# Performance work log

Hardware: AMD Instinct MI355X
Metric: run time of the kernel (lower is better)

## Reference

```python
import jax, jax.numpy as jnp
import numpy as np

N_NODES = 100000


def _gcn_norm(edge_index, num_nodes):
    # PyG gcn_norm with add_self_loops=True, symmetric normalization.
    src = jnp.concatenate([edge_index[0], jnp.arange(num_nodes)])
    dst = jnp.concatenate([edge_index[1], jnp.arange(num_nodes)])
    ones = jnp.ones(src.shape[0], dtype=jnp.float32)
    deg = jax.ops.segment_sum(ones, dst, num_segments=num_nodes)
    dinv = jnp.where(deg > 0, jax.lax.rsqrt(deg), 0.0)
    norm = dinv[src] * dinv[dst]  # [E + N]
    return src, dst, norm


def _gcn_conv(x, W, b, src, dst, norm, num_nodes):
    h = x @ W                                  # dense transform first (PyG order)
    msg = h[src] * norm[:, None]               # gather + scale, [E+N, D]
    agg = jax.ops.segment_sum(msg, dst, num_segments=num_nodes)
    return agg + b


def setup_inputs() -> dict:
    key = jax.random.key(0)
    ks = jax.random.split(key, 6)
    F_in, D, C, E = 256, 64, 47, 1200000
    x = jax.random.normal(ks[0], (N_NODES, F_in), dtype=jnp.float32)
    edge_index = jax.random.randint(ks[1], (2, E), 0, N_NODES)
    W1 = jax.random.normal(ks[2], (F_in, D), dtype=jnp.float32) * (1.0 / np.sqrt(F_in))
    b1 = jnp.zeros((D,), dtype=jnp.float32)
    W2 = jax.random.normal(ks[3], (D, C), dtype=jnp.float32) * (1.0 / np.sqrt(D))
    b2 = jnp.zeros((C,), dtype=jnp.float32)
    return {"x": x, "edge_index": edge_index, "W1": W1, "b1": b1, "W2": W2, "b2": b2}


def reference(x, edge_index, W1, b1, W2, b2):
    src, dst, norm = _gcn_norm(edge_index, N_NODES)
    h = jax.nn.relu(_gcn_conv(x, W1, b1, src, dst, norm, N_NODES))
    # dropout: eval mode (training=False) -> identity
    out = _gcn_conv(h, W2, b2, src, dst, norm, N_NODES)
    return jax.nn.log_softmax(out, axis=1)
```

## Files before the change

kernel.cpp:

```cpp
#include <hip/hip_runtime.h>
#include <math.h>

#define NN 100000
#define FIN 256
#define D1 64
#define C2 47
#define S2 48
#define PREPB 76
#define NBKT 1563
#define CAP 1024
#define EPB 4096

typedef unsigned short u16;
typedef unsigned int u32;
typedef __attribute__((ext_vector_type(8))) short short8;
typedef __attribute__((ext_vector_type(4))) float floatx4;

__device__ __forceinline__ u16 f2b(float f) {
    union { float f; unsigned u; } v; v.f = f;
    unsigned r = v.u + 0x7FFF + ((v.u >> 16) & 1);
    return (u16)(r >> 16);
}
__device__ __forceinline__ float b2f_lo(u32 p) { union { unsigned u; float f; } v; v.u = p << 16; return v.f; }
__device__ __forceinline__ float b2f_hi(u32 p) { union { unsigned u; float f; } v; v.u = p & 0xFFFF0000u; return v.f; }

__global__ __launch_bounds__(256) void k_prep_bucket(
    const float* __restrict__ W1, const float* __restrict__ W2,
    u16* __restrict__ W1t, u16* __restrict__ W2t,
    const int* __restrict__ src, const int* __restrict__ dst, int E,
    int* __restrict__ bucketCnt, u32* __restrict__ ebuf)
{
    int b = blockIdx.x;
    if (b < PREPB) {
        int i = b * 256 + threadIdx.x;
        if (i < FIN * D1) {
            int c = i >> 8, k = i & 255;
            W1t[i] = f2b(W1[k * D1 + c]);
        } else if (i < FIN * D1 + D1 * S2) {
            int j = i - FIN * D1;
            int c = j >> 6, k = j & 63;
            W2t[j] = (c < C2) ? f2b(W2[k * C2 + c]) : (u16)0;
        }
        return;
    }
    __shared__ int hist[NBKT];
    __shared__ int base[NBKT];
    const int t = threadIdx.x;
    const int blk = b - PREPB;
    for (int i = t; i < NBKT; i += 256) hist[i] = 0;
    __syncthreads();

    int e0 = blk * EPB + t;
    u32 pk[16]; int bk[16], tk[16];
    #pragma unroll
    for (int j = 0; j < 16; ++j) {
        int e = e0 + j * 256;
        bk[j] = -1;
        if (e < E) {
            int d = dst[e];
            bk[j] = d >> 6;
            pk[j] = (u32)src[e] | ((u32)(d & 63) << 17);
            tk[j] = atomicAdd(&hist[bk[j]], 1);
        }
    }
    __syncthreads();
    for (int i = t; i < NBKT; i += 256)
        base[i] = hist[i] ? atomicAdd(&bucketCnt[i], hist[i]) : 0;
    __syncthreads();
    #pragma unroll
    for (int j = 0; j < 16; ++j)
        if (bk[j] >= 0) {
            int pos = base[bk[j]] + tk[j];
            if (pos < CAP) ebuf[(size_t)bk[j] * CAP + pos] = pk[j];
        }
}

__global__ __launch_bounds__(256) void k_gemm1(
    const int* __restrict__ bucketCnt, const u32* __restrict__ ebuf,
    const float* __restrict__ x, const u16* __restrict__ W1t,
    float* __restrict__ dinv, int* __restrict__ rpg, u32* __restrict__ sortedg,
    u16* __restrict__ hs1)
{
    __shared__ short As[2][64 * 40];
    __shared__ short Bs[2][64 * 40];
    __shared__ int hist[64], cur[64];
    __shared__ float dinvs[64];
    const int b = blockIdx.x;
    const int t = threadIdx.x;
    const int bm = b * 64;

    if (t < 64) hist[t] = 0;
    __syncthreads();
    int cnt = bucketCnt[b]; if (cnt > CAP) cnt = CAP;
    const u32* eb = ebuf + (size_t)b * CAP;
    for (int i = t; i < cnt; i += 256)
        atomicAdd(&hist[(eb[i] >> 17) & 63], 1);
    __syncthreads();
    if (t < 64) {
        int h = hist[t];
        int v = h;
        #pragma unroll
        for (int off = 1; off < 64; off <<= 1) {
            int u = __shfl_up(v, off);
            if (t >= off) v += u;
        }
        cur[t] = v - h;
        rpg[(size_t)b * 64 + t] = v - h;
        float dv = rsqrtf((float)h + 1.0f);
        dinvs[t] = dv;
        dinv[bm + t] = dv;
    }
    __syncthreads();
    for (int i = t; i < cnt; i += 256) {
        u32 p = eb[i];
        int pos = atomicAdd(&cur[(p >> 17) & 63], 1);
        sortedg[(size_t)b * CAP + pos] = p & 0x1FFFF;
    }

    const int w = t >> 6, lane = t & 63;
    const int arow = t >> 2;
    const int ak0 = (t & 3) * 8;

    floatx4 acc[4] = {};
    const int gr = bm + arow;
    const bool rowok = gr < NN;
    const float* xrow = x + (size_t)(rowok ? gr : 0) * FIN + ak0;

    float4 v0 = make_float4(0.f,0.f,0.f,0.f), v1 = v0;
    if (rowok) { v0 = *(const float4*)(xrow); v1 = *(const float4*)(xrow + 4); }
    short8 wv = *(const short8*)(W1t + arow * FIN + ak0);
    {
        short8 av;
        av[0]=(short)f2b(v0.x); av[1]=(short)f2b(v0.y); av[2]=(short)f2b(v0.z); av[3]=(short)f2b(v0.w);
        av[4]=(short)f2b(v1.x); av[5]=(short)f2b(v1.y); av[6]=(short)f2b(v1.z); av[7]=(short)f2b(v1.w);
        *(short8*)(&As[0][arow * 40 + ak0]) = av;
        *(short8*)(&Bs[0][arow * 40 + ak0]) = wv;
    }
    __syncthreads();

    int cb_ = 0;
    for (int kt = 32; kt <= FIN; kt += 32) {
        const bool more = kt < FIN;
        float4 n0, n1; short8 nw;
        if (more) {
            if (rowok) { n0 = *(const float4*)(xrow + kt); n1 = *(const float4*)(xrow + kt + 4); }
            else { n0 = make_float4(0.f,0.f,0.f,0.f); n1 = n0; }
            nw = *(const short8*)(W1t + arow * FIN + kt + ak0);
        }
        short8 af = *(const short8*)(&As[cb_][(w * 16 + (lane & 15)) * 40 + (lane >> 4) * 8]);
        #pragma unroll
        for (int cb = 0; cb < 4; ++cb) {
            short8 bv = *(const short8*)(&Bs[cb_][(cb * 16 + (lane & 15)) * 40 + (lane >> 4) * 8]);
            acc[cb] = __builtin_amdgcn_mfma_f32_16x16x32_bf16(af, bv, acc[cb], 0, 0, 0);
        }
        if (!more) break;
        short8 av;
        av[0]=(short)f2b(n0.x); av[1]=(short)f2b(n0.y); av[2]=(short)f2b(n0.z); av[3]=(short)f2b(n0.w);
        av[4]=(short)f2b(n1.x); av[5]=(short)f2b(n1.y); av[6]=(short)f2b(n1.z); av[7]=(short)f2b(n1.w);
        *(short8*)(&As[cb_ ^ 1][arow * 40 + ak0]) = av;
        *(short8*)(&Bs[cb_ ^ 1][arow * 40 + ak0]) = nw;
        __syncthreads();
        cb_ ^= 1;
    }

    #pragma unroll
    for (int cb = 0; cb < 4; ++cb) {
        #pragma unroll
        for (int r = 0; r < 4; ++r) {
            int rl = w * 16 + (lane >> 4) * 4 + r;
            int grow = bm + rl;
            if (grow < NN) {
                float v = acc[cb][r] * dinvs[rl];
                hs1[(size_t)grow * D1 + cb * 16 + (lane & 15)] = f2b(v);
            }
        }
    }
}

__global__ __launch_bounds__(256) void k_gather_gemm2(
    const int* __restrict__ bucketCnt, const int* __restrict__ rpg,
    const u32* __restrict__ sortedg,
    const float* __restrict__ dinv, const u16* __restrict__ hs1,
    const float* __restrict__ b1, const u16* __restrict__ W2t,
    u16* __restrict__ hs2)
{
    __shared__ u32 sorted[CAP];
    __shared__ int rp[65];
    __shared__ short As[2][64 * 40];
    __shared__ short Bs[2][48 * 40];
    __shared__ float dinvs[64];
    __shared__ float b1s[64];
    const int t = threadIdx.x;
    const int b = blockIdx.x, bm = b * 64;
    const int w = t >> 6, lane = t & 63;
    const int g = t >> 3, l8 = t & 7;

    for (int s = t; s < 384; s += 256) {
        int kt = s / 192, rem = s - kt * 192;
        int r = rem >> 2, j = rem & 3;
        *(short8*)(&Bs[kt][r * 40 + j * 8]) =
            *(const short8*)(W2t + r * D1 + kt * 32 + j * 8);
    }
    int cnt = bucketCnt[b]; if (cnt > CAP) cnt = CAP;
    if (t < 64) { dinvs[t] = dinv[bm + t]; b1s[t] = b1[t]; rp[t] = rpg[(size_t)b * 64 + t]; }
    if (t == 0) rp[64] = cnt;
    for (int i = t; i < cnt; i += 256)
        sorted[i] = sortedg[(size_t)b * CAP + i];
    __syncthreads();

    {
        const int col = 8 * l8;
        const int kth = l8 >> 2;
        const int cs  = col & 31;
        float4 bbl = *(const float4*)(b1s + col);
        float4 bbh = *(const float4*)(b1s + col + 4);
        #pragma unroll 1
        for (int i = 0; i < 2; ++i) {
            int rl = g * 2 + i;
            int node = bm + rl;
            if (node >= NN) break;
            int beg = rp[rl], end = rp[rl + 1];
            uint4 sp = *((const uint4*)(hs1 + (size_t)node * D1) + l8);
            float a0=b2f_lo(sp.x), a1=b2f_hi(sp.x), a2=b2f_lo(sp.y), a3=b2f_hi(sp.y);
            float a4=b2f_lo(sp.z), a5=b2f_hi(sp.z), a6=b2f_lo(sp.w), a7=b2f_hi(sp.w);
            float c0=0.f,c1=0.f,c2=0.f,c3=0.f,c4=0.f,c5=0.f,c6=0.f,c7=0.f;
            int e = beg;
            for (; e + 4 <= end; e += 4) {
                int s0 = sorted[e+0], s1 = sorted[e+1], s2 = sorted[e+2], s3 = sorted[e+3];
                uint4 p0 = *((const uint4*)(hs1 + (size_t)s0 * D1) + l8);
                uint4 p1 = *((const uint4*)(hs1 + (size_t)s1 * D1) + l8);
                uint4 p2 = *((const uint4*)(hs1 + (size_t)s2 * D1) + l8);
                uint4 p3 = *((const uint4*)(hs1 + (size_t)s3 * D1) + l8);
                a0+=b2f_lo(p0.x); a1+=b2f_hi(p0.x); a2+=b2f_lo(p0.y); a3+=b2f_hi(p0.y);
                a4+=b2f_lo(p0.z); a5+=b2f_hi(p0.z); a6+=b2f_lo(p0.w); a7+=b2f_hi(p0.w);
                c0+=b2f_lo(p1.x); c1+=b2f_hi(p1.x); c2+=b2f_lo(p1.y); c3+=b2f_hi(p1.y);
                c4+=b2f_lo(p1.z); c5+=b2f_hi(p1.z); c6+=b2f_lo(p1.w); c7+=b2f_hi(p1.w);
                a0+=b2f_lo(p2.x); a1+=b2f_hi(p2.x); a2+=b2f_lo(p2.y); a3+=b2f_hi(p2.y);
                a4+=b2f_lo(p2.z); a5+=b2f_hi(p2.z); a6+=b2f_lo(p2.w); a7+=b2f_hi(p2.w);
                c0+=b2f_lo(p3.x); c1+=b2f_hi(p3.x); c2+=b2f_lo(p3.y); c3+=b2f_hi(p3.y);
                c4+=b2f_lo(p3.z); c5+=b2f_hi(p3.z); c6+=b2f_lo(p3.w); c7+=b2f_hi(p3.w);
            }
            for (; e < end; ++e) {
                uint4 p0 = *((const uint4*)(hs1 + (size_t)sorted[e] * D1) + l8);
                a0+=b2f_lo(p0.x); a1+=b2f_hi(p0.x); a2+=b2f_lo(p0.y); a3+=b2f_hi(p0.y);
                a4+=b2f_lo(p0.z); a5+=b2f_hi(p0.z); a6+=b2f_lo(p0.w); a7+=b2f_hi(p0.w);
            }
            float dd = dinvs[rl];
            float r0 = fmaxf(fmaf(dd, a0 + c0, bbl.x), 0.f);
            float r1 = fmaxf(fmaf(dd, a1 + c1, bbl.y), 0.f);
            float r2 = fmaxf(fmaf(dd, a2 + c2, bbl.z), 0.f);
            float r3 = fmaxf(fmaf(dd, a3 + c3, bbl.w), 0.f);
            float r4 = fmaxf(fmaf(dd, a4 + c4, bbh.x), 0.f);
            float r5 = fmaxf(fmaf(dd, a5 + c5, bbh.y), 0.f);
            float r6 = fmaxf(fmaf(dd, a6 + c6, bbh.z), 0.f);
            float r7 = fmaxf(fmaf(dd, a7 + c7, bbh.w), 0.f);
            short8 pk;
            pk[0]=(short)f2b(r0); pk[1]=(short)f2b(r1); pk[2]=(short)f2b(r2); pk[3]=(short)f2b(r3);
            pk[4]=(short)f2b(r4); pk[5]=(short)f2b(r5); pk[6]=(short)f2b(r6); pk[7]=(short)f2b(r7);
            *(short8*)(&As[kth][rl * 40 + cs]) = pk;
        }
    }
    __syncthreads();

    floatx4 acc2[3] = {};
    #pragma unroll
    for (int kt = 0; kt < 2; ++kt) {
        short8 af = *(const short8*)(&As[kt][(w * 16 + (lane & 15)) * 40 + (lane >> 4) * 8]);
        #pragma unroll
        for (int cb = 0; cb < 3; ++cb) {
            short8 bv = *(const short8*)(&Bs[kt][(cb * 16 + (lane & 15)) * 40 + (lane >> 4) * 8]);
            acc2[cb] = __builtin_amdgcn_mfma_f32_16x16x32_bf16(af, bv, acc2[cb], 0, 0, 0);
        }
    }

    #pragma unroll
    for (int cb = 0; cb < 3; ++cb) {
        #pragma unroll
        for (int r = 0; r < 4; ++r) {
            int rl2 = w * 16 + (lane >> 4) * 4 + r;
            int grow = bm + rl2;
            if (grow < NN) {
                float v = acc2[cb][r] * dinvs[rl2];
                hs2[(size_t)grow * S2 + cb * 16 + (lane & 15)] = f2b(v);
            }
        }
    }
}

__global__ __launch_bounds__(256) void k_gather47(
    const int* __restrict__ bucketCnt, const int* __restrict__ rpg,
    const u32* __restrict__ sortedg,
    const float* __restrict__ dinv, const u16* __restrict__ hs2,
    const float* __restrict__ b2, float* __restrict__ out)
{
    __shared__ u32 sorted[CAP];
    __shared__ int rp[65];
    __shared__ float dinvs[64];
    __shared__ float b2s[48];
    const int t = threadIdx.x;
    const int b = blockIdx.x, bm = b * 64;
    const int g = t >> 3, l8 = t & 7;

    int cnt = bucketCnt[b]; if (cnt > CAP) cnt = CAP;
    if (t < 64) { dinvs[t] = dinv[bm + t]; rp[t] = rpg[(size_t)b * 64 + t]; }
    if (t < 48) b2s[t] = (t < C2) ? b2[t] : 0.f;
    if (t == 0) rp[64] = cnt;
    for (int i = t; i < cnt; i += 256)
        sorted[i] = sortedg[(size_t)b * CAP + i];
    __syncthreads();

    const bool act = l8 < 6;
    const int lc = act ? l8 : 0;
    #pragma unroll 1
    for (int i = 0; i < 2; ++i) {
        int rl = g * 2 + i;
        int node = bm + rl;
        if (node >= NN) break;
        int beg = rp[rl], end = rp[rl + 1];
        uint4 sp = *((const uint4*)(hs2 + (size_t)node * S2) + lc);
        float a0=b2f_lo(sp.x), a1=b2f_hi(sp.x), a2=b2f_lo(sp.y), a3=b2f_hi(sp.y);
        float a4=b2f_lo(sp.z), a5=b2f_hi(sp.z), a6=b2f_lo(sp.w), a7=b2f_hi(sp.w);
        float c0=0.f,c1=0.f,c2=0.f,c3=0.f,c4=0.f,c5=0.f,c6=0.f,c7=0.f;
        int e = beg;
        for (; e + 4 <= end; e += 4) {
            int s0 = sorted[e+0], s1 = sorted[e+1], s2 = sorted[e+2], s3 = sorted[e+3];
            uint4 p0 = *((const uint4*)(hs2 + (size_t)s0 * S2) + lc);
            uint4 p1 = *((const uint4*)(hs2 + (size_t)s1 * S2) + lc);
            uint4 p2 = *((const uint4*)(hs2 + (size_t)s2 * S2) + lc);
            uint4 p3 = *((const uint4*)(hs2 + (size_t)s3 * S2) + lc);
            a0+=b2f_lo(p0.x); a1+=b2f_hi(p0.x); a2+=b2f_lo(p0.y); a3+=b2f_hi(p0.y);
            a4+=b2f_lo(p0.z); a5+=b2f_hi(p0.z); a6+=b2f_lo(p0.w); a7+=b2f_hi(p0.w);
            c0+=b2f_lo(p1.x); c1+=b2f_hi(p1.x); c2+=b2f_lo(p1.y); c3+=b2f_hi(p1.y);
            c4+=b2f_lo(p1.z); c5+=b2f_hi(p1.z); c6+=b2f_lo(p1.w); c7+=b2f_hi(p1.w);
            a0+=b2f_lo(p2.x); a1+=b2f_hi(p2.x); a2+=b2f_lo(p2.y); a3+=b2f_hi(p2.y);
            a4+=b2f_lo(p2.z); a5+=b2f_hi(p2.z); a6+=b2f_lo(p2.w); a7+=b2f_hi(p2.w);
            c0+=b2f_lo(p3.x); c1+=b2f_hi(p3.x); c2+=b2f_lo(p3.y); c3+=b2f_hi(p3.y);
            c4+=b2f_lo(p3.z); c5+=b2f_hi(p3.z); c6+=b2f_lo(p3.w); c7+=b2f_hi(p3.w);
        }
        for (; e < end; ++e) {
            uint4 p0 = *((const uint4*)(hs2 + (size_t)sorted[e] * S2) + lc);
            a0+=b2f_lo(p0.x); a1+=b2f_hi(p0.x); a2+=b2f_lo(p0.y); a3+=b2f_hi(p0.y);
            a4+=b2f_lo(p0.z); a5+=b2f_hi(p0.z); a6+=b2f_lo(p0.w); a7+=b2f_hi(p0.w);
        }
        float dd = dinvs[rl];
        float fv[8] = { a0+c0, a1+c1, a2+c2, a3+c3, a4+c4, a5+c5, a6+c6, a7+c7 };
        const int fb = 8 * lc;
        float val[8];
        float m = -INFINITY;
        #pragma unroll
        for (int k = 0; k < 8; ++k) {
            int fe = fb + k;
            bool valid = act && (fe < C2);
            val[k] = valid ? fmaf(dd, fv[k], b2s[valid ? fe : 0]) : -INFINITY;
            m = fmaxf(m, val[k]);
        }
        #pragma unroll
        for (int off = 1; off < 8; off <<= 1) m = fmaxf(m, __shfl_xor(m, off));
        float ex = 0.f;
        #pragma unroll
        for (int k = 0; k < 8; ++k)
            if (val[k] > -INFINITY) ex += expf(val[k] - m);
        #pragma unroll
        for (int off = 1; off < 8; off <<= 1) ex += __shfl_xor(ex, off);
        float ls = m + logf(ex);
        #pragma unroll
        for (int k = 0; k < 8; ++k) {
            int fe = fb + k;
            if (act && fe < C2) out[(size_t)node * C2 + fe] = val[k] - ls;
        }
    }
}

extern "C" void kernel_launch(void* const* d_in, const int* in_sizes, int n_in,
                              void* d_out, int out_size, void* d_ws, size_t ws_size,
                              hipStream_t stream) {
    const float* x  = (const float*)d_in[0];
    const int*   ei = (const int*)d_in[1];
    const float* W1 = (const float*)d_in[2];
    const float* b1 = (const float*)d_in[3];
    const float* W2 = (const float*)d_in[4];
    const float* b2 = (const float*)d_in[5];
    float* out = (float*)d_out;

    const int E = in_sizes[1] / 2;
    const int* src = ei;
    const int* dst = ei + E;

    char* ws = (char*)d_ws;
    float* dinv      = (float*)(ws);
    int*   bucketCnt = (int*)(ws + 0x80000);
    u16*   W1t       = (u16*)(ws + 0x180000);
    u16*   W2t       = (u16*)(ws + 0x189000);
    int*   rpg       = (int*)(ws + 0x190000);
    u32*   ebuf      = (u32*)(ws + 0x200000);
    u32*   sortedg   = (u32*)(ws + 0x900000);
    u16*   hs1       = (u16*)(ws + 0x1000000);
    u16*   hs2       = (u16*)(ws + 0x1E00000);

    const int nBk1 = (E + EPB - 1) / EPB;

    hipMemsetAsync(bucketCnt, 0, NBKT * sizeof(int), stream);
    k_prep_bucket<<<PREPB + nBk1, 256, 0, stream>>>(W1, W2, W1t, W2t, src, dst, E,
                                                    bucketCnt, ebuf);
    k_gemm1<<<NBKT, 256, 0, stream>>>(bucketCnt, ebuf, x, W1t, dinv, rpg, sortedg, hs1);
    k_gather_gemm2<<<NBKT, 256, 0, stream>>>(bucketCnt, rpg, sortedg, dinv, hs1, b1, W2t, hs2);
    k_gather47<<<NBKT, 256, 0, stream>>>(bucketCnt, rpg, sortedg, dinv, hs2, b2, out);
}
```

Before: 124.3 us.

## Overlap edge binning with GEMM1 and move degree scaling into a sort kernel

The edge bucket scatter now runs in the same launch as the dense x@W1 GEMM, so the two independent phases can overlap across CUs. The memset is folded into the weight-prep kernel. Because the GEMM no longer waits on degrees, it writes unscaled h1 and a new sort/scale kernel rescales it by dinv. Downstream kernels recompute dinv from row-pointer counts instead of reading a dinv array. The cost is an extra launch and an extra read and write pass over h1.

```diff
diff --git a/kernel.cpp b/kernel.cpp
--- a/kernel.cpp
+++ b/kernel.cpp
@@ -6,7 +6,6 @@
 #define D1 64
 #define C2 47
 #define S2 48
-#define PREPB 76
 #define NBKT 1563
 #define CAP 1024
 #define EPB 4096
@@ -23,100 +22,72 @@
 }
 __device__ __forceinline__ float b2f_lo(u32 p) { union { unsigned u; float f; } v; v.u = p << 16; return v.f; }
 __device__ __forceinline__ float b2f_hi(u32 p) { union { unsigned u; float f; } v; v.u = p & 0xFFFF0000u; return v.f; }
-
-__global__ __launch_bounds__(256) void k_prep_bucket(
+__device__ __forceinline__ u32 scale2(u32 pair, float dd) {
+    return (u32)f2b(dd * b2f_lo(pair)) | ((u32)f2b(dd * b2f_hi(pair)) << 16);
+}
+
+__global__ __launch_bounds__(256) void k_pre(
     const float* __restrict__ W1, const float* __restrict__ W2,
-    u16* __restrict__ W1t, u16* __restrict__ W2t,
-    const int* __restrict__ src, const int* __restrict__ dst, int E,
-    int* __restrict__ bucketCnt, u32* __restrict__ ebuf)
+    u16* __restrict__ W1t, u16* __restrict__ W2t, int* __restrict__ bucketCnt)
 {
-    int b = blockIdx.x;
-    if (b < PREPB) {
-        int i = b * 256 + threadIdx.x;
-        if (i < FIN * D1) {
-            int c = i >> 8, k = i & 255;
-            W1t[i] = f2b(W1[k * D1 + c]);
-        } else if (i < FIN * D1 + D1 * S2) {
-            int j = i - FIN * D1;
-            int c = j >> 6, k = j & 63;
-            W2t[j] = (c < C2) ? f2b(W2[k * C2 + c]) : (u16)0;
-        }
-        return;
-    }
-    __shared__ int hist[NBKT];
-    __shared__ int base[NBKT];
-    const int t = threadIdx.x;
-    const int blk = b - PREPB;
-    for (int i = t; i < NBKT; i += 256) hist[i] = 0;
-    __syncthreads();
-
-    int e0 = blk * EPB + t;
-    u32 pk[16]; int bk[16], tk[16];
-    #pragma unroll
-    for (int j = 0; j < 16; ++j) {
-        int e = e0 + j * 256;
-        bk[j] = -1;
-        if (e < E) {
-            int d = dst[e];
-            bk[j] = d >> 6;
-            pk[j] = (u32)src[e] | ((u32)(d & 63) << 17);
-            tk[j] = atomicAdd(&hist[bk[j]], 1);
-        }
-    }
-    __syncthreads();
-    for (int i = t; i < NBKT; i += 256)
-        base[i] = hist[i] ? atomicAdd(&bucketCnt[i], hist[i]) : 0;
-    __syncthreads();
-    #pragma unroll
-    for (int j = 0; j < 16; ++j)
-        if (bk[j] >= 0) {
-            int pos = base[bk[j]] + tk[j];
-            if (pos < CAP) ebuf[(size_t)bk[j] * CAP + pos] = pk[j];
-        }
-}
-
-__global__ __launch_bounds__(256) void k_gemm1(
-    const int* __restrict__ bucketCnt, const u32* __restrict__ ebuf,
+    int i = blockIdx.x * 256 + threadIdx.x;
+    if (i < FIN * D1) {
+        int c = i >> 8, k = i & 255;
+        W1t[i] = f2b(W1[k * D1 + c]);
+    } else if (i < FIN * D1 + D1 * S2) {
+        int j = i - FIN * D1;
+        int c = j >> 6, k = j & 63;
+        W2t[j] = (c < C2) ? f2b(W2[k * C2 + c]) : (u16)0;
+    } else {
+        int z = i - (FIN * D1 + D1 * S2);
+        if (z < NBKT) bucketCnt[z] = 0;
+    }
+}
+
+__global__ __launch_bounds__(256) void k_bin_gemm1(
+    const int* __restrict__ src, const int* __restrict__ dst, int E, int nScat,
+    int* __restrict__ bucketCnt, u32* __restrict__ ebuf,
     const float* __restrict__ x, const u16* __restrict__ W1t,
-    float* __restrict__ dinv, int* __restrict__ rpg, u32* __restrict__ sortedg,
-    u16* __restrict__ hs1)
+    u16* __restrict__ h1u)
 {
-    __shared__ short As[2][64 * 40];
-    __shared__ short Bs[2][64 * 40];
-    __shared__ int hist[64], cur[64];
-    __shared__ float dinvs[64];
+    __shared__ __align__(16) char smraw[20480];
     const int b = blockIdx.x;
     const int t = threadIdx.x;
-    const int bm = b * 64;
-
-    if (t < 64) hist[t] = 0;
-    __syncthreads();
-    int cnt = bucketCnt[b]; if (cnt > CAP) cnt = CAP;
-    const u32* eb = ebuf + (size_t)b * CAP;
-    for (int i = t; i < cnt; i += 256)
-        atomicAdd(&hist[(eb[i] >> 17) & 63], 1);
-    __syncthreads();
-    if (t < 64) {
-        int h = hist[t];
-        int v = h;
-        #pragma unroll
-        for (int off = 1; off < 64; off <<= 1) {
-            int u = __shfl_up(v, off);
-            if (t >= off) v += u;
-        }
-        cur[t] = v - h;
-        rpg[(size_t)b * 64 + t] = v - h;
-        float dv = rsqrtf((float)h + 1.0f);
-        dinvs[t] = dv;
-        dinv[bm + t] = dv;
-    }
-    __syncthreads();
-    for (int i = t; i < cnt; i += 256) {
-        u32 p = eb[i];
-        int pos = atomicAdd(&cur[(p >> 17) & 63], 1);
-        sortedg[(size_t)b * CAP + pos] = p & 0x1FFFF;
-    }
-
+
+    if (b < nScat) {
+        int* hist = (int*)smraw;
+        int* base = (int*)(smraw + 6256);
+        for (int i = t; i < NBKT; i += 256) hist[i] = 0;
+        __syncthreads();
+        int e0 = b * EPB + t;
+        u32 pk[16]; int bk[16], tk[16];
+        #pragma unroll
+        for (int j = 0; j < 16; ++j) {
+            int e = e0 + j * 256;
+            bk[j] = -1;
+            if (e < E) {
+                int d = dst[e];
+                bk[j] = d >> 6;
+                pk[j] = (u32)src[e] | ((u32)(d & 63) << 17);
+                tk[j] = atomicAdd(&hist[bk[j]], 1);
+            }
+        }
+        __syncthreads();
+        for (int i = t; i < NBKT; i += 256)
+            base[i] = hist[i] ? atomicAdd(&bucketCnt[i], hist[i]) : 0;
+        __syncthreads();
+        #pragma unroll
+        for (int j = 0; j < 16; ++j)
+            if (bk[j] >= 0) {
+                int pos = base[bk[j]] + tk[j];
+                if (pos < CAP) ebuf[(size_t)bk[j] * CAP + pos] = pk[j];
+            }
+        return;
+    }
+
+    short (*As)[2560] = (short(*)[2560])(smraw);
+    short (*Bs)[2560] = (short(*)[2560])(smraw + 10240);
+    const int bm = (b - nScat) * 64;
     const int w = t >> 6, lane = t & 63;
     const int arow = t >> 2;
     const int ak0 = (t & 3) * 8;
@@ -167,20 +138,72 @@
     for (int cb = 0; cb < 4; ++cb) {
         #pragma unroll
         for (int r = 0; r < 4; ++r) {
-            int rl = w * 16 + (lane >> 4) * 4 + r;
-            int grow = bm + rl;
-            if (grow < NN) {
-                float v = acc[cb][r] * dinvs[rl];
-                hs1[(size_t)grow * D1 + cb * 16 + (lane & 15)] = f2b(v);
-            }
+            int grow = bm + w * 16 + (lane >> 4) * 4 + r;
+            if (grow < NN)
+                h1u[(size_t)grow * D1 + cb * 16 + (lane & 15)] = f2b(acc[cb][r]);
+        }
+    }
+}
+
+__global__ __launch_bounds__(256) void k_sort_scale(
+    const int* __restrict__ bucketCnt, const u32* __restrict__ ebuf,
+    int* __restrict__ rpg, u32* __restrict__ sortedg,
+    const u16* __restrict__ h1u, u16* __restrict__ hs1)
+{
+    __shared__ int hist[64], cur[64];
+    __shared__ float dinvs[64];
+    const int b = blockIdx.x, t = threadIdx.x, bm = b * 64;
+
+    if (t < 64) hist[t] = 0;
+    __syncthreads();
+    int cnt = bucketCnt[b]; if (cnt > CAP) cnt = CAP;
+    const u32* eb = ebuf + (size_t)b * CAP;
+    u32 p[4];
+    #pragma unroll
+    for (int j = 0; j < 4; ++j) {
+        int e = t + j * 256;
+        p[j] = 0xFFFFFFFFu;
+        if (e < cnt) { p[j] = eb[e]; atomicAdd(&hist[(p[j] >> 17) & 63], 1); }
+    }
+    __syncthreads();
+    if (t < 64) {
+        int h = hist[t];
+        int v = h;
+        #pragma unroll
+        for (int off = 1; off < 64; off <<= 1) {
+            int u = __shfl_up(v, off);
+            if (t >= off) v += u;
+        }
+        cur[t] = v - h;
+        rpg[(size_t)b * 64 + t] = v - h;
+        dinvs[t] = rsqrtf((float)h + 1.0f);
+    }
+    __syncthreads();
+    #pragma unroll
+    for (int j = 0; j < 4; ++j)
+        if (p[j] != 0xFFFFFFFFu) {
+            int pos = atomicAdd(&cur[(p[j] >> 17) & 63], 1);
+            sortedg[(size_t)b * CAP + pos] = p[j] & 0x1FFFF;
+        }
+
+    const uint4* hb = (const uint4*)(h1u + (size_t)bm * D1);
+    uint4* ob = (uint4*)(hs1 + (size_t)bm * D1);
+    #pragma unroll
+    for (int j = 0; j < 2; ++j) {
+        int idx = t + j * 256;
+        int row = idx >> 3;
+        if (bm + row < NN) {
+            uint4 v = hb[idx];
+            float dd = dinvs[row];
+            ob[idx] = make_uint4(scale2(v.x, dd), scale2(v.y, dd),
+                                 scale2(v.z, dd), scale2(v.w, dd));
         }
     }
 }
 
 __global__ __launch_bounds__(256) void k_gather_gemm2(
     const int* __restrict__ bucketCnt, const int* __restrict__ rpg,
-    const u32* __restrict__ sortedg,
-    const float* __restrict__ dinv, const u16* __restrict__ hs1,
+    const u32* __restrict__ sortedg, const u16* __restrict__ hs1,
     const float* __restrict__ b1, const u16* __restrict__ W2t,
     u16* __restrict__ hs2)
 {
@@ -188,7 +211,6 @@
     __shared__ int rp[65];
     __shared__ short As[2][64 * 40];
     __shared__ short Bs[2][48 * 40];
-    __shared__ float dinvs[64];
     __shared__ float b1s[64];
     const int t = threadIdx.x;
     const int b = blockIdx.x, bm = b * 64;
@@ -202,7 +224,7 @@
             *(const short8*)(W2t + r * D1 + kt * 32 + j * 8);
     }
     int cnt = bucketCnt[b]; if (cnt > CAP) cnt = CAP;
-    if (t < 64) { dinvs[t] = dinv[bm + t]; b1s[t] = b1[t]; rp[t] = rpg[(size_t)b * 64 + t]; }
+    if (t < 64) { b1s[t] = b1[t]; rp[t] = rpg[(size_t)b * 64 + t]; }
     if (t == 0) rp[64] = cnt;
     for (int i = t; i < cnt; i += 256)
         sorted[i] = sortedg[(size_t)b * CAP + i];
@@ -220,6 +242,7 @@
             int node = bm + rl;
             if (node >= NN) break;
             int beg = rp[rl], end = rp[rl + 1];
+            float dd = rsqrtf((float)(end - beg) + 1.0f);
             uint4 sp = *((const uint4*)(hs1 + (size_t)node * D1) + l8);
             float a0=b2f_lo(sp.x), a1=b2f_hi(sp.x), a2=b2f_lo(sp.y), a3=b2f_hi(sp.y);
             float a4=b2f_lo(sp.z), a5=b2f_hi(sp.z), a6=b2f_lo(sp.w), a7=b2f_hi(sp.w);
@@ -245,7 +268,6 @@
                 a0+=b2f_lo(p0.x); a1+=b2f_hi(p0.x); a2+=b2f_lo(p0.y); a3+=b2f_hi(p0.y);
                 a4+=b2f_lo(p0.z); a5+=b2f_hi(p0.z); a6+=b2f_lo(p0.w); a7+=b2f_hi(p0.w);
             }
-            float dd = dinvs[rl];
             float r0 = fmaxf(fmaf(dd, a0 + c0, bbl.x), 0.f);
             float r1 = fmaxf(fmaf(dd, a1 + c1, bbl.y), 0.f);
             float r2 = fmaxf(fmaf(dd, a2 + c2, bbl.z), 0.f);
@@ -274,13 +296,14 @@
     }
 
     #pragma unroll
-    for (int cb = 0; cb < 3; ++cb) {
-        #pragma unroll
-        for (int r = 0; r < 4; ++r) {
-            int rl2 = w * 16 + (lane >> 4) * 4 + r;
-            int grow = bm + rl2;
-            if (grow < NN) {
-                float v = acc2[cb][r] * dinvs[rl2];
+    for (int r = 0; r < 4; ++r) {
+        int rl2 = w * 16 + (lane >> 4) * 4 + r;
+        int grow = bm + rl2;
+        if (grow < NN) {
+            float dd2 = rsqrtf((float)(rp[rl2 + 1] - rp[rl2]) + 1.0f);
+            #pragma unroll
+            for (int cb = 0; cb < 3; ++cb) {
+                float v = acc2[cb][r] * dd2;
                 hs2[(size_t)grow * S2 + cb * 16 + (lane & 15)] = f2b(v);
             }
         }
@@ -289,20 +312,18 @@
 
 __global__ __launch_bounds__(256) void k_gather47(
     const int* __restrict__ bucketCnt, const int* __restrict__ rpg,
-    const u32* __restrict__ sortedg,
-    const float* __restrict__ dinv, const u16* __restrict__ hs2,
+    const u32* __restrict__ sortedg, const u16* __restrict__ hs2,
     const float* __restrict__ b2, float* __restrict__ out)
 {
     __shared__ u32 sorted[CAP];
     __shared__ int rp[65];
-    __shared__ float dinvs[64];
     __shared__ float b2s[48];
     const int t = threadIdx.x;
     const int b = blockIdx.x, bm = b * 64;
     const int g = t >> 3, l8 = t & 7;
 
     int cnt = bucketCnt[b]; if (cnt > CAP) cnt = CAP;
-    if (t < 64) { dinvs[t] = dinv[bm + t]; rp[t] = rpg[(size_t)b * 64 + t]; }
+    if (t < 64) rp[t] = rpg[(size_t)b * 64 + t];
     if (t < 48) b2s[t] = (t < C2) ? b2[t] : 0.f;
     if (t == 0) rp[64] = cnt;
     for (int i = t; i < cnt; i += 256)
@@ -317,6 +338,7 @@
         int node = bm + rl;
         if (node >= NN) break;
         int beg = rp[rl], end = rp[rl + 1];
+        float dd = rsqrtf((float)(end - beg) + 1.0f);
         uint4 sp = *((const uint4*)(hs2 + (size_t)node * S2) + lc);
         float a0=b2f_lo(sp.x), a1=b2f_hi(sp.x), a2=b2f_lo(sp.y), a3=b2f_hi(sp.y);
         float a4=b2f_lo(sp.z), a5=b2f_hi(sp.z), a6=b2f_lo(sp.w), a7=b2f_hi(sp.w);
@@ -342,7 +364,6 @@
             a0+=b2f_lo(p0.x); a1+=b2f_hi(p0.x); a2+=b2f_lo(p0.y); a3+=b2f_hi(p0.y);
             a4+=b2f_lo(p0.z); a5+=b2f_hi(p0.z); a6+=b2f_lo(p0.w); a7+=b2f_hi(p0.w);
         }
-        float dd = dinvs[rl];
         float fv[8] = { a0+c0, a1+c1, a2+c2, a3+c3, a4+c4, a5+c5, a6+c6, a7+c7 };
         const int fb = 8 * lc;
         float val[8];
@@ -387,22 +408,23 @@
     const int* dst = ei + E;
 
     char* ws = (char*)d_ws;
-    float* dinv      = (float*)(ws);
-    int*   bucketCnt = (int*)(ws + 0x80000);
-    u16*   W1t       = (u16*)(ws + 0x180000);
-    u16*   W2t       = (u16*)(ws + 0x189000);
-    int*   rpg       = (int*)(ws + 0x190000);
-    u32*   ebuf      = (u32*)(ws + 0x200000);
-    u32*   sortedg   = (u32*)(ws + 0x900000);
-    u16*   hs1       = (u16*)(ws + 0x1000000);
-    u16*   hs2       = (u16*)(ws + 0x1E00000);
+    int*   bucketCnt = (int*)(ws);
+    u16*   W1t       = (u16*)(ws + 0x10000);
+    u16*   W2t       = (u16*)(ws + 0x19000);
+    int*   rpg       = (int*)(ws + 0x20000);
+    u32*   ebuf      = (u32*)(ws + 0x100000);
+    u32*   sortedg   = (u32*)(ws + 0x800000);
+    u16*   h1u       = (u16*)(ws + 0xF00000);
+    u16*   hs1       = (u16*)(ws + 0x1C00000);
+    u16*   hs2       = (u16*)(ws + 0x2900000);
 
     const int nBk1 = (E + EPB - 1) / EPB;
-
-    hipMemsetAsync(bucketCnt, 0, NBKT * sizeof(int), stream);
-    k_prep_bucket<<<PREPB + nBk1, 256, 0, stream>>>(W1, W2, W1t, W2t, src, dst, E,
-                                                    bucketCnt, ebuf);
-    k_gemm1<<<NBKT, 256, 0, stream>>>(bucketCnt, ebuf, x, W1t, dinv, rpg, sortedg, hs1);
-    k_gather_gemm2<<<NBKT, 256, 0, stream>>>(bucketCnt, rpg, sortedg, dinv, hs1, b1, W2t, hs2);
-    k_gather47<<<NBKT, 256, 0, stream>>>(bucketCnt, rpg, sortedg, dinv, hs2, b2, out);
-}
+    const int preB = (FIN * D1 + D1 * S2 + NBKT + 255) / 256;
+
+    k_pre<<<preB, 256, 0, stream>>>(W1, W2, W1t, W2t, bucketCnt);
+    k_bin_gemm1<<<nBk1 + NBKT, 256, 0, stream>>>(src, dst, E, nBk1,
+                                                 bucketCnt, ebuf, x, W1t, h1u);
+    k_sort_scale<<<NBKT, 256, 0, stream>>>(bucketCnt, ebuf, rpg, sortedg, h1u, hs1);
+    k_gather_gemm2<<<NBKT, 256, 0, stream>>>(bucketCnt, rpg, sortedg, hs1, b1, W2t, hs2);
+    k_gather47<<<NBKT, 256, 0, stream>>>(bucketCnt, rpg, sortedg, hs2, b2, out);
+}
```

Result: faster. 116.9 us, median of 2 (-6.0%).
